# Kernel tuning notes

Measured on AMD Instinct MI355X. Metric: run time of the kernel, lower is better.

The kernel has to match this reference:

```python
import jax, jax.numpy as jnp
import numpy as np

DIM = 1024
CTX_DIM = 768
HEADS = 16
D_HEAD = 64
INNER = HEADS * D_HEAD  # 1024
EPS = 1e-5


def _layernorm(x, g, b):
    mu = jnp.mean(x, axis=-1, keepdims=True)
    var = jnp.mean(jnp.square(x - mu), axis=-1, keepdims=True)
    return (x - mu) * jax.lax.rsqrt(var + EPS) * g + b


def setup_inputs() -> dict:
    key = jax.random.key(0)
    ks = jax.random.split(key, 8)
    s = lambda fan_in: 1.0 / np.sqrt(fan_in)
    return {
        "x": jax.random.normal(ks[0], (4, 2048, DIM), dtype=jnp.float32),
        "context": jax.random.normal(ks[1], (4, 2048, CTX_DIM), dtype=jnp.float32),
        "norm_g": jnp.ones((DIM,), jnp.float32),
        "norm_b": jnp.zeros((DIM,), jnp.float32),
        "normc_g": jnp.ones((CTX_DIM,), jnp.float32),
        "normc_b": jnp.zeros((CTX_DIM,), jnp.float32),
        # Linear weights stored [in, out] so y = x @ W (bias=False as in module)
        "Wq": jax.random.uniform(ks[2], (DIM, INNER), jnp.float32, -s(DIM), s(DIM)),
        "Wk": jax.random.uniform(ks[3], (CTX_DIM, INNER), jnp.float32, -s(CTX_DIM), s(CTX_DIM)),
        "Wv": jax.random.uniform(ks[4], (CTX_DIM, INNER), jnp.float32, -s(CTX_DIM), s(CTX_DIM)),
        "Wo": jax.random.uniform(ks[5], (INNER, DIM), jnp.float32, -s(INNER), s(INNER)),
    }


def reference(x, context, norm_g, norm_b, normc_g, normc_b, Wq, Wk, Wv, Wo):
    b, n, _ = x.shape
    m = context.shape[1]
    xn = _layernorm(x, norm_g, norm_b)
    cn = _layernorm(context, normc_g, normc_b)
    # project and split heads: b n (h d) -> b h n d
    split = lambda t, L: t.reshape(b, L, HEADS, D_HEAD).transpose(0, 2, 1, 3)
    q = split(xn @ Wq, n)
    k = split(cn @ Wk, m)
    v = split(cn @ Wv, m)
    sim = jnp.einsum('bhid,bhjd->bhij', q, k) / np.sqrt(D_HEAD)
    attn = jax.nn.softmax(sim, axis=-1)  # dropout p=0 (eval): identity
    out = jnp.einsum('bhij,bhjd->bhid', attn, v)
    out = out.transpose(0, 2, 1, 3).reshape(b, n, INNER)
    return out @ Wo
```

## Files before the change

kernel.cpp:

```cpp
#include <hip/hip_runtime.h>
#include <hip/hip_bf16.h>
#include <stdint.h>

#define TOK 8192
#define NQ 2048
#define DIMX 1024
#define CTXD 768

typedef __attribute__((ext_vector_type(8))) short short8;
typedef __attribute__((ext_vector_type(4))) float f32x4;
typedef __attribute__((ext_vector_type(2))) unsigned int u32x2;

typedef __attribute__((address_space(3))) uint32_t lds_u32_t;
typedef const __attribute__((address_space(1))) uint32_t glb_u32_t;

__device__ __forceinline__ void gld_lds16(const void* g, void* l) {
  __builtin_amdgcn_global_load_lds((glb_u32_t*)g, (lds_u32_t*)l, 16, 0, 0);
}

__device__ __forceinline__ uint16_t f2bf(float f) {
  union { float f; uint32_t u; } v; v.f = f;
  uint32_t r = v.u + 0x7fffu + ((v.u >> 16) & 1u);
  return (uint16_t)(r >> 16);
}

__device__ __forceinline__ uint32_t cvt_pk_bf16(float lo, float hi) {
  uint32_t d;
  asm("v_cvt_pk_bf16_f32 %0, %1, %2" : "=v"(d) : "v"(lo), "v"(hi));
  return d;
}

__device__ __forceinline__ float fexp2(float x) {
#if __has_builtin(__builtin_amdgcn_exp2f)
  return __builtin_amdgcn_exp2f(x);
#else
  float d;
  asm volatile("v_exp_f32 %0, %1\n\ts_nop 1" : "=v"(d) : "v"(x));
  return d;
#endif
}

__global__ __launch_bounds__(256)
void ln_tr_kernel(const float* __restrict__ x, const float* __restrict__ gx,
                  const float* __restrict__ bx,
                  const float* __restrict__ c, const float* __restrict__ gc,
                  const float* __restrict__ bc,
                  uint16_t* __restrict__ xn, uint16_t* __restrict__ cn,
                  const float* __restrict__ W0, const float* __restrict__ W1,
                  const float* __restrict__ W2, const float* __restrict__ W3,
                  uint16_t* __restrict__ T0, uint16_t* __restrict__ T1,
                  uint16_t* __restrict__ T2, uint16_t* __restrict__ T3) {
  int bid = blockIdx.x;
  int tid = threadIdx.x;
  if (bid >= 2 * TOK) {
    int t = bid - 2 * TOK;
    int z = t >> 10, rem = t & 1023;
    const float* W = (z == 0) ? W0 : (z == 1) ? W1 : (z == 2) ? W2 : W3;
    uint16_t* WT   = (z == 0) ? T0 : (z == 1) ? T1 : (z == 2) ? T2 : T3;
    int K = (z == 1 || z == 2) ? CTXD : DIMX;
    const int N = DIMX;
    int c0 = (rem & 31) * 32, r0 = (rem >> 5) * 32;
    if (r0 >= K) return;
    __shared__ float tb[32][33];
    int tx = tid & 31, ty = tid >> 5;
#pragma unroll
    for (int i = 0; i < 4; i++)
      tb[ty + 8*i][tx] = W[(size_t)(r0 + ty + 8*i) * N + c0 + tx];
    __syncthreads();
#pragma unroll
    for (int i = 0; i < 4; i++)
      WT[(size_t)(c0 + ty + 8*i) * K + r0 + tx] = f2bf(tb[tx][ty + 8*i]);
    return;
  }
  int row = bid;
  const float *src, *g, *bb; uint16_t* dst; int COLS;
  if (row < TOK) { src = x; g = gx; bb = bx; dst = xn; COLS = DIMX; }
  else { row -= TOK; src = c; g = gc; bb = bc; dst = cn; COLS = CTXD; }
  bool act = tid * 4 < COLS;
  float4 v = make_float4(0.f, 0.f, 0.f, 0.f);
  if (act) v = *(const float4*)(src + (size_t)row * COLS + tid * 4);
  float s1 = v.x + v.y + v.z + v.w;
  float s2 = v.x*v.x + v.y*v.y + v.z*v.z + v.w*v.w;
#pragma unroll
  for (int off = 1; off < 64; off <<= 1) {
    s1 += __shfl_xor(s1, off);
    s2 += __shfl_xor(s2, off);
  }
  __shared__ float sm[2][4];
  int w = tid >> 6;
  if ((tid & 63) == 0) { sm[0][w] = s1; sm[1][w] = s2; }
  __syncthreads();
  float t1 = sm[0][0] + sm[0][1] + sm[0][2] + sm[0][3];
  float t2 = sm[1][0] + sm[1][1] + sm[1][2] + sm[1][3];
  float mu = t1 / COLS;
  float var = t2 / COLS - mu * mu;
  float rs = rsqrtf(var + 1e-5f);
  if (act) {
    float4 gv = *(const float4*)(g + tid * 4);
    float4 bv = *(const float4*)(bb + tid * 4);
    uint32_t lo = (uint32_t)f2bf((v.x - mu) * rs * gv.x + bv.x) |
                  ((uint32_t)f2bf((v.y - mu) * rs * gv.y + bv.y) << 16);
    uint32_t hi = (uint32_t)f2bf((v.z - mu) * rs * gv.z + bv.z) |
                  ((uint32_t)f2bf((v.w - mu) * rs * gv.w + bv.w) << 16);
    uint2 o; o.x = lo; o.y = hi;
    *(uint2*)(dst + (size_t)row * COLS + tid * 4) = o;
  }
}

__device__ __forceinline__ void gemm_block(
    const uint16_t* __restrict__ A, const uint16_t* __restrict__ BT,
    void* __restrict__ C, int N, int K, float oscale,
    int out_bf16, int permc, int m0, int n0,
    uint16_t* Al, uint16_t* Bl, int tid) {
  int l = tid & 63, w = tid >> 6;
  int g = l >> 4, r = l & 15;
  int wm = w >> 1, wn = w & 1;
  f32x4 acc[4][4] = {};
  int srow = tid >> 3, sslot = tid & 7;

  for (int kt = 0; kt < K; kt += 64) {
    __syncthreads();
#pragma unroll
    for (int c = 0; c < 4; c++) {
      int row = c * 32 + srow;
      int ksrc = (sslot * 8) ^ ((row & 7) << 3);
      gld_lds16(A + (size_t)(m0 + row) * K + kt + ksrc, Al + (c * 256 + w * 64) * 8);
    }
#pragma unroll
    for (int c = 0; c < 4; c++) {
      int row = c * 32 + srow;
      int ksrc = (sslot * 8) ^ ((row & 7) << 3);
      gld_lds16(BT + (size_t)(n0 + row) * K + kt + ksrc, Bl + (c * 256 + w * 64) * 8);
    }
    __syncthreads();
#pragma unroll
    for (int kk = 0; kk < 2; kk++) {
      int kb2 = (kk * 32 + g * 8) * 2;
      short8 af[4], bfr[4];
#pragma unroll
      for (int mf = 0; mf < 4; mf++) {
        int row = wm * 64 + mf * 16 + r;
        af[mf] = *(const short8*)((const char*)Al + row * 128 + (kb2 ^ ((row & 7) << 4)));
      }
#pragma unroll
      for (int nf = 0; nf < 4; nf++) {
        int row = wn * 64 + nf * 16 + r;
        bfr[nf] = *(const short8*)((const char*)Bl + row * 128 + (kb2 ^ ((row & 7) << 4)));
      }
#pragma unroll
      for (int mf = 0; mf < 4; mf++)
#pragma unroll
        for (int nf = 0; nf < 4; nf++)
          acc[mf][nf] = __builtin_amdgcn_mfma_f32_16x16x32_bf16(af[mf], bfr[nf], acc[mf][nf], 0, 0, 0);
    }
  }
#pragma unroll
  for (int mf = 0; mf < 4; mf++) {
#pragma unroll
    for (int i = 0; i < 4; i++) {
      size_t row = (size_t)m0 + wm * 64 + mf * 16 + g * 4 + i;
      if (permc) {
        int pbase = ((r >> 3) << 4) | (((r >> 2) & 1) << 3) | (r & 3);
        uint16_t* cb = (uint16_t*)C + row * N + n0 + wn * 64;
        cb[pbase +  0] = f2bf(acc[mf][0][i]);
        cb[pbase +  4] = f2bf(acc[mf][1][i]);
        cb[pbase + 32] = f2bf(acc[mf][2][i]);
        cb[pbase + 36] = f2bf(acc[mf][3][i]);
      } else {
#pragma unroll
        for (int nf = 0; nf < 4; nf++) {
          int col = n0 + wn * 64 + nf * 16 + r;
          float val = acc[mf][nf][i] * oscale;
          if (out_bf16) ((uint16_t*)C)[row * N + col] = f2bf(val);
          else          ((float*)C)[row * N + col] = val;
        }
      }
    }
  }
}

__global__ __launch_bounds__(256)
void gemm_proj3_kernel(const uint16_t* __restrict__ xn, const uint16_t* __restrict__ cn,
                       const uint16_t* __restrict__ WqT, const uint16_t* __restrict__ WkT,
                       const uint16_t* __restrict__ WvT,
                       uint16_t* __restrict__ Qs, uint16_t* __restrict__ Ks,
                       uint16_t* __restrict__ VTs, float qscale) {
  __shared__ __align__(16) uint16_t Al[128 * 64];
  __shared__ __align__(16) uint16_t Bl[128 * 64];
  int flat = blockIdx.x;
  flat = (flat & 7) * 192 + (flat >> 3);
  const uint16_t* A; const uint16_t* BT; uint16_t* C;
  int N, K, permc, m0, n0;
  float osc = 1.f;
  if (flat < 512) {
    A = xn; BT = WqT; C = Qs; N = DIMX; K = DIMX; permc = 0; osc = qscale;
    n0 = (flat & 7) * 128; m0 = (flat >> 3) * 128;
  } else if (flat < 1024) {
    int f = flat - 512;
    A = cn; BT = WkT; C = Ks; N = DIMX; K = CTXD; permc = 0;
    n0 = (f & 7) * 128; m0 = (f >> 3) * 128;
  } else {
    int f = flat - 1024;
    A = WvT; BT = cn; C = VTs; N = TOK; K = CTXD; permc = 1;
    n0 = (f & 63) * 128; m0 = (f >> 6) * 128;
  }
  gemm_block(A, BT, C, N, K, osc, 1, permc, m0, n0, Al, Bl, threadIdx.x);
}

__global__ __launch_bounds__(256)
void gemm_out_kernel(const uint16_t* __restrict__ A, const uint16_t* __restrict__ BT,
                     float* __restrict__ C, int M, int N, int K) {
  __shared__ __align__(16) uint16_t Al[128 * 64];
  __shared__ __align__(16) uint16_t Bl[128 * 64];
  int flat = blockIdx.y * gridDim.x + blockIdx.x;
  int nwg = gridDim.x * gridDim.y;
  flat = (flat & 7) * (nwg >> 3) + (flat >> 3);
  int bx = flat & (gridDim.x - 1);
  int by = flat / gridDim.x;
  gemm_block(A, BT, C, N, K, 1.f, 0, 0, by * 128, bx * 128, Al, Bl, threadIdx.x);
}

__global__ __launch_bounds__(256, 2)
void attn_kernel(const uint16_t* __restrict__ Q, const uint16_t* __restrict__ Kp,
                 const uint16_t* __restrict__ VT, uint16_t* __restrict__ O) {
  __shared__ __align__(16) uint16_t Kl[64 * 64];
  __shared__ __align__(16) uint16_t Vl[64 * 64];
  int tid = threadIdx.x;
  int l = tid & 63, w = tid >> 6;
  int g = l >> 4, r = l & 15;
  int flat = blockIdx.y * 8 + blockIdx.x;
  flat = (flat & 7) * 64 + (flat >> 3);
  int q0 = (flat & 7) * 256;
  int bh = flat >> 3, b = bh >> 4, h = bh & 15;

  short8 qa[4][2];
#pragma unroll
  for (int qb = 0; qb < 4; qb++) {
    const uint16_t* qptr = Q + (size_t)(b * NQ + q0 + w * 64 + qb * 16 + r) * DIMX + h * 64;
    qa[qb][0] = *(const short8*)(qptr + g * 8);
    qa[qb][1] = *(const short8*)(qptr + 32 + g * 8);
  }

  float lpart[4] = {0.f, 0.f, 0.f, 0.f};
  f32x4 oacc[4][4] = {};

  const uint16_t* kbase = Kp + (size_t)(b * NQ) * DIMX + h * 64;
  const uint16_t* vbase = VT + (size_t)(h * 64) * TOK + b * NQ;
  int srow = tid >> 3, sslot = tid & 7;

  for (int kv0 = 0; kv0 < NQ; kv0 += 64) {
    __syncthreads();
#pragma unroll
    for (int c = 0; c < 2; c++) {
      int key = c * 32 + srow;
      int dsrc = (sslot * 8) ^ ((key & 7) << 3);
      gld_lds16(kbase + (size_t)(kv0 + key) * DIMX + dsrc, Kl + (c * 256 + w * 64) * 8);
    }
#pragma unroll
    for (int c = 0; c < 2; c++) {
      int d = c * 32 + srow;
      int ksrc = (sslot * 8) ^ ((d & 7) << 3);
      gld_lds16(vbase + (size_t)d * TOK + kv0 + ksrc, Vl + (c * 256 + w * 64) * 8);
    }
    __syncthreads();

    f32x4 sc[4][4] = {};
    __builtin_amdgcn_s_setprio(1);
#pragma unroll
    for (int kk = 0; kk < 2; kk++) {
      int kb2 = (kk * 32 + g * 8) * 2;
#pragma unroll
      for (int c = 0; c < 4; c++) {
        int row = c * 16 + r;
        short8 kf = *(const short8*)((const char*)Kl + row * 128 + (kb2 ^ ((row & 7) << 4)));
#pragma unroll
        for (int qb = 0; qb < 4; qb++)
          sc[qb][c] = __builtin_amdgcn_mfma_f32_16x16x32_bf16(kf, qa[qb][kk], sc[qb][c], 0, 0, 0);
      }
    }
    __builtin_amdgcn_s_setprio(0);

    short8 pa[4][2];
#pragma unroll
    for (int qb = 0; qb < 4; qb++) {
      float pe[4][4];
#pragma unroll
      for (int c = 0; c < 4; c++)
#pragma unroll
        for (int i = 0; i < 4; i++) {
          pe[c][i] = fexp2(sc[qb][c][i]);
          lpart[qb] += pe[c][i];
        }
#pragma unroll
      for (int kk = 0; kk < 2; kk++) {
        union { uint32_t u[4]; short8 s; } pk;
        pk.u[0] = cvt_pk_bf16(pe[kk * 2][0], pe[kk * 2][1]);
        pk.u[1] = cvt_pk_bf16(pe[kk * 2][2], pe[kk * 2][3]);
        pk.u[2] = cvt_pk_bf16(pe[kk * 2 + 1][0], pe[kk * 2 + 1][1]);
        pk.u[3] = cvt_pk_bf16(pe[kk * 2 + 1][2], pe[kk * 2 + 1][3]);
        pa[qb][kk] = pk.s;
      }
    }

    __builtin_amdgcn_s_setprio(1);
#pragma unroll
    for (int kk = 0; kk < 2; kk++) {
#pragma unroll
      for (int c = 0; c < 4; c++) {
        int row = c * 16 + r;
        short8 vf = *(const short8*)((const char*)Vl + row * 128 + (((kk * 32 + g * 8) * 2) ^ ((row & 7) << 4)));
#pragma unroll
        for (int qb = 0; qb < 4; qb++)
          oacc[qb][c] = __builtin_amdgcn_mfma_f32_16x16x32_bf16(pa[qb][kk], vf, oacc[qb][c], 0, 0, 0);
      }
    }
    __builtin_amdgcn_s_setprio(0);
  }

#pragma unroll
  for (int qb = 0; qb < 4; qb++) {
    lpart[qb] += __shfl_xor(lpart[qb], 16);
    lpart[qb] += __shfl_xor(lpart[qb], 32);
  }

#pragma unroll
  for (int qb = 0; qb < 4; qb++) {
    uint16_t* obase = O + (size_t)(b * NQ + q0 + w * 64 + qb * 16) * DIMX + h * 64;
#pragma unroll
    for (int i = 0; i < 4; i++) {
      float li = __shfl(lpart[qb], g * 4 + i);
      float inv = 1.f / li;
#pragma unroll
      for (int c = 0; c < 4; c++)
        obase[(size_t)(g * 4 + i) * DIMX + c * 16 + r] = f2bf(oacc[qb][c][i] * inv);
    }
  }
}

extern "C" void kernel_launch(void* const* d_in, const int* in_sizes, int n_in,
                              void* d_out, int out_size, void* d_ws, size_t ws_size,
                              hipStream_t stream) {
  (void)in_sizes; (void)n_in; (void)out_size; (void)ws_size;
  const float* x       = (const float*)d_in[0];
  const float* ctx     = (const float*)d_in[1];
  const float* norm_g  = (const float*)d_in[2];
  const float* norm_b  = (const float*)d_in[3];
  const float* normc_g = (const float*)d_in[4];
  const float* normc_b = (const float*)d_in[5];
  const float* Wq      = (const float*)d_in[6];
  const float* Wk      = (const float*)d_in[7];
  const float* Wv      = (const float*)d_in[8];
  const float* Wo      = (const float*)d_in[9];

  char* p = (char*)d_ws;
  uint16_t* xn  = (uint16_t*)p; p += (size_t)TOK * DIMX * 2;
  uint16_t* cn  = (uint16_t*)p; p += (size_t)TOK * CTXD * 2;
  uint16_t* WqT = (uint16_t*)p; p += (size_t)DIMX * DIMX * 2;
  uint16_t* WkT = (uint16_t*)p; p += (size_t)DIMX * CTXD * 2;
  uint16_t* WvT = (uint16_t*)p; p += (size_t)DIMX * CTXD * 2;
  uint16_t* WoT = (uint16_t*)p; p += (size_t)DIMX * DIMX * 2;
  uint16_t* Qs  = (uint16_t*)p; p += (size_t)TOK * DIMX * 2;
  uint16_t* Ks  = (uint16_t*)p; p += (size_t)TOK * DIMX * 2;
  uint16_t* VTs = (uint16_t*)p; p += (size_t)DIMX * TOK * 2;
  uint16_t* AO  = (uint16_t*)p; p += (size_t)TOK * DIMX * 2;

  ln_tr_kernel<<<2 * TOK + 4096, 256, 0, stream>>>(
      x, norm_g, norm_b, ctx, normc_g, normc_b, xn, cn,
      Wq, Wk, Wv, Wo, WqT, WkT, WvT, WoT);

  const float qscale = 0.125f * 1.44269504088896340736f;
  gemm_proj3_kernel<<<1536, 256, 0, stream>>>(xn, cn, WqT, WkT, WvT, Qs, Ks, VTs, qscale);

  attn_kernel<<<dim3(8, 64), 256, 0, stream>>>(Qs, Ks, VTs, AO);

  gemm_out_kernel<<<dim3(DIMX/128, TOK/128), 256, 0, stream>>>(AO, WoT, (float*)d_out, TOK, DIMX, DIMX);
}
```

Before: 178.2 us.

## Double-buffer K/V tiles in attention kernel to overlap loads with MFMA

Splits the K and V shared-memory tiles into two buffers. The next tile's global-to-LDS loads are issued before computing on the current tile, with one barrier per iteration at the end, so the load latency can hide behind the QK and PV MFMAs. Per-block LDS doubles, from 16KB to 32KB, which still fits the occupancy of 2 blocks per CU. The barrier at the end of the iteration is expected to wait on the async LDS loads (vmcnt) before the next tile is read.

```diff
diff --git a/kernel.cpp b/kernel.cpp
--- a/kernel.cpp
+++ b/kernel.cpp
@@ -223,8 +223,8 @@
 __global__ __launch_bounds__(256, 2)
 void attn_kernel(const uint16_t* __restrict__ Q, const uint16_t* __restrict__ Kp,
                  const uint16_t* __restrict__ VT, uint16_t* __restrict__ O) {
-  __shared__ __align__(16) uint16_t Kl[64 * 64];
-  __shared__ __align__(16) uint16_t Vl[64 * 64];
+  __shared__ __align__(16) uint16_t Kl[2][64 * 64];
+  __shared__ __align__(16) uint16_t Vl[2][64 * 64];
   int tid = threadIdx.x;
   int l = tid & 63, w = tid >> 6;
   int g = l >> 4, r = l & 15;
@@ -247,22 +247,30 @@
   const uint16_t* kbase = Kp + (size_t)(b * NQ) * DIMX + h * 64;
   const uint16_t* vbase = VT + (size_t)(h * 64) * TOK + b * NQ;
   int srow = tid >> 3, sslot = tid & 7;
-
-  for (int kv0 = 0; kv0 < NQ; kv0 += 64) {
-    __syncthreads();
-#pragma unroll
-    for (int c = 0; c < 2; c++) {
-      int key = c * 32 + srow;
-      int dsrc = (sslot * 8) ^ ((key & 7) << 3);
-      gld_lds16(kbase + (size_t)(kv0 + key) * DIMX + dsrc, Kl + (c * 256 + w * 64) * 8);
-    }
-#pragma unroll
-    for (int c = 0; c < 2; c++) {
-      int d = c * 32 + srow;
-      int ksrc = (sslot * 8) ^ ((d & 7) << 3);
-      gld_lds16(vbase + (size_t)d * TOK + kv0 + ksrc, Vl + (c * 256 + w * 64) * 8);
-    }
-    __syncthreads();
+  int krow0 = srow, krow1 = 32 + srow;
+  int kd0 = (sslot * 8) ^ ((krow0 & 7) << 3);
+  int kd1 = (sslot * 8) ^ ((krow1 & 7) << 3);
+
+  gld_lds16(kbase + (size_t)krow0 * DIMX + kd0, &Kl[0][0] + (0 * 256 + w * 64) * 8);
+  gld_lds16(kbase + (size_t)krow1 * DIMX + kd1, &Kl[0][0] + (1 * 256 + w * 64) * 8);
+  gld_lds16(vbase + (size_t)krow0 * TOK + kd0, &Vl[0][0] + (0 * 256 + w * 64) * 8);
+  gld_lds16(vbase + (size_t)krow1 * TOK + kd1, &Vl[0][0] + (1 * 256 + w * 64) * 8);
+  __syncthreads();
+
+  const int NT = NQ / 64;
+  for (int t = 0; t < NT; t++) {
+    int cur = t & 1;
+    if (t + 1 < NT) {
+      int kvn = (t + 1) * 64;
+      uint16_t* kd = &Kl[cur ^ 1][0];
+      uint16_t* vd = &Vl[cur ^ 1][0];
+      gld_lds16(kbase + (size_t)(kvn + krow0) * DIMX + kd0, kd + (0 * 256 + w * 64) * 8);
+      gld_lds16(kbase + (size_t)(kvn + krow1) * DIMX + kd1, kd + (1 * 256 + w * 64) * 8);
+      gld_lds16(vbase + (size_t)krow0 * TOK + kvn + kd0, vd + (0 * 256 + w * 64) * 8);
+      gld_lds16(vbase + (size_t)krow1 * TOK + kvn + kd1, vd + (1 * 256 + w * 64) * 8);
+    }
+    const char* Kb = (const char*)&Kl[cur][0];
+    const char* Vb = (const char*)&Vl[cur][0];
 
     f32x4 sc[4][4] = {};
     __builtin_amdgcn_s_setprio(1);
@@ -272,7 +280,7 @@
 #pragma unroll
       for (int c = 0; c < 4; c++) {
         int row = c * 16 + r;
-        short8 kf = *(const short8*)((const char*)Kl + row * 128 + (kb2 ^ ((row & 7) << 4)));
+        short8 kf = *(const short8*)(Kb + row * 128 + (kb2 ^ ((row & 7) << 4)));
 #pragma unroll
         for (int qb = 0; qb < 4; qb++)
           sc[qb][c] = __builtin_amdgcn_mfma_f32_16x16x32_bf16(kf, qa[qb][kk], sc[qb][c], 0, 0, 0);
@@ -308,13 +316,15 @@
 #pragma unroll
       for (int c = 0; c < 4; c++) {
         int row = c * 16 + r;
-        short8 vf = *(const short8*)((const char*)Vl + row * 128 + (((kk * 32 + g * 8) * 2) ^ ((row & 7) << 4)));
+        short8 vf = *(const short8*)(Vb + row * 128 + (((kk * 32 + g * 8) * 2) ^ ((row & 7) << 4)));
 #pragma unroll
         for (int qb = 0; qb < 4; qb++)
           oacc[qb][c] = __builtin_amdgcn_mfma_f32_16x16x32_bf16(pa[qb][kk], vf, oacc[qb][c], 0, 0, 0);
       }
     }
     __builtin_amdgcn_s_setprio(0);
+
+    __syncthreads();
   }
 
 #pragma unroll
```

Result: no change. 179.7 us (+0.8%).
